# Kernel tuning notes

Measured on AMD Instinct MI355X. Metric: run time of the kernel, lower is better.

## Reference

```python
import jax, jax.numpy as jnp
import numpy as np

N, F, E = 100000, 128, 1600000


def setup_inputs() -> dict:
    key = jax.random.key(0)
    ks = jax.random.split(key, 10)
    s = 1.0 / np.sqrt(F)
    return {
        "x": jax.random.normal(ks[0], (N, F), jnp.float32),
        "edge_index": jax.random.randint(ks[1], (2, E), 0, N),
        "edge_weight": jax.random.uniform(ks[2], (E,), jnp.float32),
        # EvolveGCNO initial weight (1, F, F) -> squeezed to (F, F)
        "initial_weight": jax.random.normal(ks[3], (F, F), jnp.float32) * s,
        # torch.nn.GRU(F, F) params, gate order (r, z, n)
        "gru_w_ih": jax.random.uniform(ks[4], (3 * F, F), jnp.float32, -s, s),
        "gru_w_hh": jax.random.uniform(ks[5], (3 * F, F), jnp.float32, -s, s),
        "gru_b_ih": jax.random.uniform(ks[6], (3 * F,), jnp.float32, -s, s),
        "gru_b_hh": jax.random.uniform(ks[7], (3 * F,), jnp.float32, -s, s),
        # Linear(F, 1)
        "lin_w": jax.random.uniform(ks[8], (1, F), jnp.float32, -s, s),
        "lin_b": jax.random.uniform(ks[9], (1,), jnp.float32, -s, s),
    }


def _evolve_weight(W0, w_ih, w_hh, b_ih, b_hh):
    # One GRU step: input = W0 rows (batch=F), hidden = W0 rows (first call of EvolveGCNO)
    gi = W0 @ w_ih.T + b_ih  # (F, 3F)
    gh = W0 @ w_hh.T + b_hh
    i_r, i_z, i_n = jnp.split(gi, 3, axis=-1)
    h_r, h_z, h_n = jnp.split(gh, 3, axis=-1)
    r = jax.nn.sigmoid(i_r + h_r)
    z = jax.nn.sigmoid(i_z + h_z)
    n = jnp.tanh(i_n + r * h_n)
    return (1.0 - z) * n + z * W0  # (F, F)


def reference(x, edge_index, edge_weight, initial_weight, gru_w_ih, gru_w_hh,
              gru_b_ih, gru_b_hh, lin_w, lin_b):
    W = _evolve_weight(initial_weight, gru_w_ih, gru_w_hh, gru_b_ih, gru_b_hh)
    n_nodes = x.shape[0]
    row, col = edge_index[0], edge_index[1]  # source, target
    # gcn_norm: add self loops (weight 1), sym-normalize D^-1/2 (A+I) D^-1/2
    loop = jnp.arange(n_nodes)
    row = jnp.concatenate([row, loop])
    col = jnp.concatenate([col, loop])
    w = jnp.concatenate([edge_weight, jnp.ones((n_nodes,), x.dtype)])
    deg = jax.ops.segment_sum(w, col, num_segments=n_nodes)
    dinv = jnp.where(deg > 0, jax.lax.rsqrt(deg), 0.0)
    norm = dinv[row] * w * dinv[col]  # (E+N,)
    xw = x @ W  # (N, F)
    # gather at sources, weighted scatter-add at targets
    h = jax.ops.segment_sum(norm[:, None] * xw[row], col, num_segments=n_nodes)
    h = jax.nn.relu(h)
    return (h @ lin_w.T + lin_b)[:, 0]  # (N,)
```

## Files before the change

kernel.cpp:

```cpp
#include <hip/hip_runtime.h>

#define F 128
#define DEG_SCALE 16777216.0f
#define DEG_INV   (1.0f / 16777216.0f)
#define BUCK_BITS 7
#define BUCK_COLS 128
#define CAP 2304
#define EPT 8

typedef _Float16 half8 __attribute__((ext_vector_type(8)));
typedef float f32x4 __attribute__((ext_vector_type(4)));
typedef float f32x2 __attribute__((ext_vector_type(2)));

__global__ __launch_bounds__(256) void init_kernel(
    int* __restrict__ cursor, int NZ, int NBUK,
    const float* __restrict__ W0, const float* __restrict__ wih,
    const float* __restrict__ whh, const float* __restrict__ bih,
    const float* __restrict__ bhh, _Float16* __restrict__ WTh,
    int* __restrict__ offs, int N, int total) {
  __shared__ float w0row[2][F];
  int b = blockIdx.x;
  if (b < NZ) {
    int i = b * 256 + threadIdx.x;
    if (i < NBUK) cursor[i] = 0;
    if (b == 0 && threadIdx.x == 0) offs[N] = total;
    return;
  }
  int half = threadIdx.x >> 7;
  int j = threadIdx.x & 127;
  int i = (b - NZ) * 2 + half;
  w0row[half][j] = W0[i * F + j];
  __syncthreads();
  float ar = 0, az = 0, an = 0, br = 0, bz = 0, bn = 0;
  const float* wi_r = wih + (size_t)j * F;
  const float* wi_z = wih + (size_t)(j + F) * F;
  const float* wi_n = wih + (size_t)(j + 2 * F) * F;
  const float* wh_r = whh + (size_t)j * F;
  const float* wh_z = whh + (size_t)(j + F) * F;
  const float* wh_n = whh + (size_t)(j + 2 * F) * F;
#pragma unroll 4
  for (int k = 0; k < F; ++k) {
    float a = w0row[half][k];
    ar = fmaf(a, wi_r[k], ar);
    az = fmaf(a, wi_z[k], az);
    an = fmaf(a, wi_n[k], an);
    br = fmaf(a, wh_r[k], br);
    bz = fmaf(a, wh_z[k], bz);
    bn = fmaf(a, wh_n[k], bn);
  }
  float gr = ar + bih[j] + br + bhh[j];
  float gz = az + bih[j + F] + bz + bhh[j + F];
  float r = 1.f / (1.f + expf(-gr));
  float z = 1.f / (1.f + expf(-gz));
  float n = tanhf(an + bih[j + 2 * F] + r * (bn + bhh[j + 2 * F]));
  float v = (1.f - z) * n + z * w0row[half][j];
  WTh[j * F + i] = (_Float16)v;
}

__global__ __launch_bounds__(256) void gemm_bin(
    const float* __restrict__ x, const _Float16* __restrict__ WT,
    _Float16* __restrict__ xwh, int N, int NG,
    const int* __restrict__ erow, const int* __restrict__ ecol,
    const float* __restrict__ ew, int* __restrict__ cursor,
    uint2* __restrict__ binned, int E, int NBUK, int NBIN) {
  __shared__ int cnt_base[2048];
  int bi = blockIdx.x;
  if (bi % 3 == 2) {
    int bb = bi / 3;
    if (bb >= NBIN) return;
    int* cnt = cnt_base;
    int* base = cnt_base + 1024;
    int tid = threadIdx.x;
    for (int u = tid; u < 1024; u += 256) cnt[u] = 0;
    __syncthreads();
    int e0 = bb * (256 * EPT) + tid;
    int cc[EPT];
    int lrank[EPT];
#pragma unroll
    for (int k = 0; k < EPT; ++k) {
      int e = e0 + k * 256;
      if (e < E) {
        cc[k] = ecol[e];
        lrank[k] = atomicAdd(&cnt[cc[k] >> BUCK_BITS], 1);
      } else cc[k] = -1;
    }
    __syncthreads();
    for (int u = tid; u < NBUK; u += 256) {
      int cu = cnt[u];
      base[u] = cu ? atomicAdd(&cursor[u], cu) : 0;
    }
    __syncthreads();
#pragma unroll
    for (int k = 0; k < EPT; ++k) {
      if (cc[k] >= 0) {
        int e = e0 + k * 256;
        int bk = cc[k] >> BUCK_BITS;
        int pos = base[bk] + lrank[k];
        if (pos < CAP) {
          unsigned cl = (unsigned)(cc[k] & (BUCK_COLS - 1));
          binned[(size_t)bk * CAP + pos] =
              make_uint2((unsigned)erow[e] | (cl << 17), __float_as_uint(ew[e]));
        }
      }
    }
    return;
  }
  int g = (bi / 3) * 2 + (bi % 3);
  if (g >= NG) return;
  int t = threadIdx.x;
  int lane = t & 63, wave = t >> 6;
  int ln = lane & 15, q = lane >> 4;
  int rowb = g * 64 + wave * 16;
  int i = rowb + ln;
  int iclamp = (i < N) ? i : N - 1;
  const float* xp = x + (size_t)iclamp * F + q * 8;

  half8 a[4];
#pragma unroll
  for (int tt = 0; tt < 4; ++tt) {
    float4 v0 = *(const float4*)(xp + 32 * tt);
    float4 v1 = *(const float4*)(xp + 32 * tt + 4);
    half8 av;
    av[0] = (_Float16)v0.x; av[1] = (_Float16)v0.y;
    av[2] = (_Float16)v0.z; av[3] = (_Float16)v0.w;
    av[4] = (_Float16)v1.x; av[5] = (_Float16)v1.y;
    av[6] = (_Float16)v1.z; av[7] = (_Float16)v1.w;
    a[tt] = av;
  }

  f32x4 acc[8];
#pragma unroll
  for (int nt = 0; nt < 8; ++nt) acc[nt] = (f32x4){0.f, 0.f, 0.f, 0.f};

#pragma unroll
  for (int nt = 0; nt < 8; ++nt) {
#pragma unroll
    for (int tt = 0; tt < 4; ++tt) {
      half8 bfrag = *(const half8*)&WT[(size_t)(nt * 16 + ln) * F + tt * 32 + q * 8];
      acc[nt] = __builtin_amdgcn_mfma_f32_16x16x32_f16(a[tt], bfrag, acc[nt], 0, 0, 0);
    }
  }

#pragma unroll
  for (int nt = 0; nt < 8; ++nt) {
#pragma unroll
    for (int r = 0; r < 4; ++r) {
      int rowi = rowb + q * 4 + r;
      if (rowi < N) xwh[(size_t)rowi * F + nt * 16 + ln] = (_Float16)acc[nt][r];
    }
  }
}

__global__ __launch_bounds__(256) void csr_deg(
    const uint2* __restrict__ binned, const int* __restrict__ cursor,
    int* __restrict__ offs, float* __restrict__ dinv, int N, int NBUK) {
  __shared__ unsigned long long acc[BUCK_COLS];
  __shared__ int sc[BUCK_COLS];
  __shared__ int wsum[4];
  int b = blockIdx.x;
  int tid = threadIdx.x;
  if (tid < BUCK_COLS) acc[tid] = 0ull;
  int partial = 0;
  for (int i = tid; i < b; i += 256) partial += cursor[i];
#pragma unroll
  for (int m = 32; m; m >>= 1) partial += __shfl_xor(partial, m);
  if ((tid & 63) == 0) wsum[tid >> 6] = partial;
  __syncthreads();
  int bstart = b * BUCK_COLS + wsum[0] + wsum[1] + wsum[2] + wsum[3];

  int cnt = cursor[b];
  if (cnt > CAP) cnt = CAP;
  const uint2* src = binned + (size_t)b * CAP;
  for (int i = tid; i < cnt; i += 256) {
    uint2 rec = src[i];
    int cl = rec.x >> 17;
    unsigned fx = (unsigned)(__uint_as_float(rec.y) * DEG_SCALE);
    atomicAdd(&acc[cl], ((unsigned long long)1 << 32) | (unsigned long long)fx);
  }
  __syncthreads();
  int node0 = b * BUCK_COLS;
  int cvt1 = 0;
  if (tid < BUCK_COLS) {
    unsigned long long pk = acc[tid];
    int node = node0 + tid;
    if (node < N) {
      cvt1 = (int)(pk >> 32) + 1;
      float deg = (float)(unsigned)(pk & 0xffffffffull) * DEG_INV;
      float dv = rsqrtf(deg + 1.0f);
      dinv[node] = dv;
    }
    sc[tid] = cvt1;
  }
  __syncthreads();
  for (int off = 1; off < BUCK_COLS; off <<= 1) {
    int xv = 0;
    if (tid < BUCK_COLS && tid >= off) xv = sc[tid - off];
    __syncthreads();
    if (tid < BUCK_COLS) sc[tid] += xv;
    __syncthreads();
  }
  if (tid < BUCK_COLS) {
    int node = node0 + tid;
    if (node < N) offs[node] = bstart + sc[tid] - cvt1;
  }
}

__global__ __launch_bounds__(256) void csr_pairs(
    const uint2* __restrict__ binned, const int* __restrict__ cursor,
    const int* __restrict__ offs, const float* __restrict__ dinv,
    uint2* __restrict__ pairs, int N, int NBUK) {
  __shared__ float dinvL[BUCK_COLS];
  __shared__ int wbase[BUCK_COLS];
  int b = blockIdx.x;
  int tid = threadIdx.x;
  int node0 = b * BUCK_COLS;
  if (tid < BUCK_COLS) {
    int node = node0 + tid;
    if (node < N) {
      int o = offs[node];
      float dv = dinv[node];
      dinvL[tid] = dv;
      wbase[tid] = o + 1;
      pairs[o] = make_uint2((unsigned)node << 8, __float_as_uint(dv * dv));
    }
  }
  __syncthreads();
  int cnt = cursor[b];
  if (cnt > CAP) cnt = CAP;
  const uint2* src = binned + (size_t)b * CAP;
  for (int i = tid; i < cnt; i += 256) {
    uint2 rec = src[i];
    int cl = rec.x >> 17;
    unsigned r = rec.x & 0x1ffffu;
    float wp = (__uint_as_float(rec.y) * dinvL[cl]) * dinv[r];
    int pos = atomicAdd(&wbase[cl], 1);
    pairs[pos] = make_uint2(r << 8, __float_as_uint(wp));
  }
}

__global__ __launch_bounds__(256) void gather_out(
    const uint2* __restrict__ pairs, const int* __restrict__ offs,
    const char* __restrict__ xwb, const float* __restrict__ linw,
    const float* __restrict__ linb, float* __restrict__ out, int N) {
  int wave = threadIdx.x >> 6;
  int lane = threadIdx.x & 63;
  int node = blockIdx.x * 4 + wave;
  if (node >= N) return;
  int c = lane & 15;
  int q = lane >> 4;

  const char* xb = xwb + (c << 4);
  f32x2 acc[4];
#pragma unroll
  for (int j = 0; j < 4; ++j) acc[j] = (f32x2){0.f, 0.f};

  int start = offs[node], end = offs[node + 1];
  for (int it = start + q; it < end; it += 16) {
    int i1 = (it + 4 < end) ? it + 4 : it;
    int i2 = (it + 8 < end) ? it + 8 : it;
    int i3 = (it + 12 < end) ? it + 12 : it;
    uint2 p0 = pairs[it];
    uint2 p1 = pairs[i1];
    uint2 p2 = pairs[i2];
    uint2 p3 = pairs[i3];
    float n0 = __uint_as_float(p0.y);
    float n1 = (it + 4 < end) ? __uint_as_float(p1.y) : 0.f;
    float n2 = (it + 8 < end) ? __uint_as_float(p2.y) : 0.f;
    float n3 = (it + 12 < end) ? __uint_as_float(p3.y) : 0.f;
    half8 x0 = *(const half8*)(xb + p0.x);
    half8 x1 = *(const half8*)(xb + p1.x);
    half8 x2 = *(const half8*)(xb + p2.x);
    half8 x3 = *(const half8*)(xb + p3.x);
    f32x2 nv0 = {n0, n0}, nv1 = {n1, n1}, nv2 = {n2, n2}, nv3 = {n3, n3};
#pragma unroll
    for (int j = 0; j < 4; ++j) {
      f32x2 v; v[0] = (float)x0[2 * j]; v[1] = (float)x0[2 * j + 1];
      acc[j] += nv0 * v;
    }
#pragma unroll
    for (int j = 0; j < 4; ++j) {
      f32x2 v; v[0] = (float)x1[2 * j]; v[1] = (float)x1[2 * j + 1];
      acc[j] += nv1 * v;
    }
#pragma unroll
    for (int j = 0; j < 4; ++j) {
      f32x2 v; v[0] = (float)x2[2 * j]; v[1] = (float)x2[2 * j + 1];
      acc[j] += nv2 * v;
    }
#pragma unroll
    for (int j = 0; j < 4; ++j) {
      f32x2 v; v[0] = (float)x3[2 * j]; v[1] = (float)x3[2 * j + 1];
      acc[j] += nv3 * v;
    }
  }

  float a8[8];
#pragma unroll
  for (int j = 0; j < 8; ++j) a8[j] = acc[j >> 1][j & 1];
#pragma unroll
  for (int j = 0; j < 8; ++j) {
    a8[j] += __shfl_xor(a8[j], 16);
    a8[j] += __shfl_xor(a8[j], 32);
  }

  const float4* lw4 = (const float4*)linw;
  float4 la = lw4[c * 2];
  float4 lb = lw4[c * 2 + 1];
  float p = fmaxf(a8[0], 0.f) * la.x + fmaxf(a8[1], 0.f) * la.y +
            fmaxf(a8[2], 0.f) * la.z + fmaxf(a8[3], 0.f) * la.w +
            fmaxf(a8[4], 0.f) * lb.x + fmaxf(a8[5], 0.f) * lb.y +
            fmaxf(a8[6], 0.f) * lb.z + fmaxf(a8[7], 0.f) * lb.w;
#pragma unroll
  for (int m = 8; m; m >>= 1) p += __shfl_xor(p, m);

  if (lane == 0) out[node] = p + linb[0];
}

extern "C" void kernel_launch(void* const* d_in, const int* in_sizes, int n_in,
                              void* d_out, int out_size, void* d_ws, size_t ws_size,
                              hipStream_t stream) {
  const float* x    = (const float*)d_in[0];
  const int*   ei   = (const int*)d_in[1];
  const float* ew   = (const float*)d_in[2];
  const float* W0   = (const float*)d_in[3];
  const float* wih  = (const float*)d_in[4];
  const float* whh  = (const float*)d_in[5];
  const float* bih  = (const float*)d_in[6];
  const float* bhh  = (const float*)d_in[7];
  const float* linw = (const float*)d_in[8];
  const float* linb = (const float*)d_in[9];

  int N = in_sizes[0] / F;
  int E = in_sizes[2];
  const int* row = ei;
  const int* col = ei + E;
  int NBUK = (N + BUCK_COLS - 1) / BUCK_COLS;
  int total = E + N;

  char* p = (char*)d_ws;
  auto alloc = [&](size_t bytes) {
    char* q = p;
    p += (bytes + 255) & ~(size_t)255;
    return q;
  };
  _Float16* WTh    = (_Float16*)alloc((size_t)F * F * 2);
  int*      cursor = (int*)alloc((size_t)NBUK * 4);
  float*    dinv   = (float*)alloc((size_t)N * 4);
  int*      offs   = (int*)alloc(((size_t)N + 1) * 4);
  uint2*    binned = (uint2*)alloc((size_t)NBUK * CAP * 8);
  uint2*    pairs  = (uint2*)alloc(((size_t)total + 16) * 8);
  _Float16* xwh    = (_Float16*)alloc((size_t)N * F * 2);

  int NZ = (NBUK + 255) / 256;
  init_kernel<<<NZ + 64, 256, 0, stream>>>(cursor, NZ, NBUK, W0, wih, whh, bih, bhh,
                                           WTh, offs, N, total);

  int NG = (N + 63) / 64;
  int NBIN = (E + 256 * EPT - 1) / (256 * EPT);
  int half_g = (NG + 1) / 2;
  int G3 = NBIN > half_g ? NBIN : half_g;
  gemm_bin<<<3 * G3, 256, 0, stream>>>(x, WTh, xwh, N, NG, row, col, ew, cursor,
                                       binned, E, NBUK, NBIN);

  csr_deg<<<NBUK, 256, 0, stream>>>(binned, cursor, offs, dinv, N, NBUK);
  csr_pairs<<<NBUK, 256, 0, stream>>>(binned, cursor, offs, dinv, pairs, N, NBUK);

  gather_out<<<(N + 3) / 4, 256, 0, stream>>>(pairs, offs, (const char*)xwh,
                                              linw, linb, (float*)d_out, N);
}
```

Baseline: 267.8 us.

## Fuse degree accumulation into gemm_bin via global atomics and co-schedule GEMM with binning

```diff
diff --git a/kernel.cpp b/kernel.cpp
--- a/kernel.cpp
+++ b/kernel.cpp
@@ -6,14 +6,15 @@
 #define BUCK_BITS 7
 #define BUCK_COLS 128
 #define CAP 2304
-#define EPT 8
+#define EPB 2048
 
 typedef _Float16 half8 __attribute__((ext_vector_type(8)));
 typedef float f32x4 __attribute__((ext_vector_type(4)));
 typedef float f32x2 __attribute__((ext_vector_type(2)));
 
 __global__ __launch_bounds__(256) void init_kernel(
-    int* __restrict__ cursor, int NZ, int NBUK,
+    int* __restrict__ cursor, unsigned long long* __restrict__ deg64,
+    int NZ, int NBUK,
     const float* __restrict__ W0, const float* __restrict__ wih,
     const float* __restrict__ whh, const float* __restrict__ bih,
     const float* __restrict__ bhh, _Float16* __restrict__ WTh,
@@ -22,6 +23,7 @@
   int b = blockIdx.x;
   if (b < NZ) {
     int i = b * 256 + threadIdx.x;
+    if (i < N) deg64[i] = 0ull;
     if (i < NBUK) cursor[i] = 0;
     if (b == 0 && threadIdx.x == 0) offs[N] = total;
     return;
@@ -57,109 +59,111 @@
   WTh[j * F + i] = (_Float16)v;
 }
 
-__global__ __launch_bounds__(256) void gemm_bin(
+__global__ __launch_bounds__(512) void gemm_bin(
     const float* __restrict__ x, const _Float16* __restrict__ WT,
-    _Float16* __restrict__ xwh, int N, int NG,
+    _Float16* __restrict__ xwh, int N,
     const int* __restrict__ erow, const int* __restrict__ ecol,
     const float* __restrict__ ew, int* __restrict__ cursor,
-    uint2* __restrict__ binned, int E, int NBUK, int NBIN) {
-  __shared__ int cnt_base[2048];
+    unsigned long long* __restrict__ deg64, uint2* __restrict__ binned,
+    int E, int NBUK) {
+  __shared__ int cnt[1024];
+  __shared__ int base[1024];
   int bi = blockIdx.x;
-  if (bi % 3 == 2) {
-    int bb = bi / 3;
-    if (bb >= NBIN) return;
-    int* cnt = cnt_base;
-    int* base = cnt_base + 1024;
-    int tid = threadIdx.x;
-    for (int u = tid; u < 1024; u += 256) cnt[u] = 0;
-    __syncthreads();
-    int e0 = bb * (256 * EPT) + tid;
-    int cc[EPT];
-    int lrank[EPT];
-#pragma unroll
-    for (int k = 0; k < EPT; ++k) {
-      int e = e0 + k * 256;
-      if (e < E) {
-        cc[k] = ecol[e];
-        lrank[k] = atomicAdd(&cnt[cc[k] >> BUCK_BITS], 1);
-      } else cc[k] = -1;
-    }
-    __syncthreads();
-    for (int u = tid; u < NBUK; u += 256) {
-      int cu = cnt[u];
-      base[u] = cu ? atomicAdd(&cursor[u], cu) : 0;
-    }
-    __syncthreads();
-#pragma unroll
-    for (int k = 0; k < EPT; ++k) {
-      if (cc[k] >= 0) {
-        int e = e0 + k * 256;
-        int bk = cc[k] >> BUCK_BITS;
-        int pos = base[bk] + lrank[k];
-        if (pos < CAP) {
-          unsigned cl = (unsigned)(cc[k] & (BUCK_COLS - 1));
-          binned[(size_t)bk * CAP + pos] =
-              make_uint2((unsigned)erow[e] | (cl << 17), __float_as_uint(ew[e]));
-        }
+  int tid = threadIdx.x;
+
+  int e0 = bi * EPB + tid;
+  int cc[4];
+  unsigned rr[4];
+  float wv[4];
+#pragma unroll
+  for (int k = 0; k < 4; ++k) {
+    int e = e0 + k * 512;
+    if (e < E) {
+      cc[k] = ecol[e];
+      rr[k] = (unsigned)erow[e];
+      wv[k] = ew[e];
+    } else cc[k] = -1;
+  }
+#pragma unroll
+  for (int k = 0; k < 4; ++k) {
+    if (cc[k] >= 0) {
+      unsigned fx = (unsigned)(wv[k] * DEG_SCALE);
+      atomicAdd(&deg64[cc[k]],
+                ((unsigned long long)1 << 32) | (unsigned long long)fx);
+    }
+  }
+  for (int u = tid; u < 1024; u += 512) cnt[u] = 0;
+
+  int lane = tid & 63, wave = tid >> 6;
+  int ln = lane & 15, q = lane >> 4;
+  int rowb0 = bi * 128;
+  if (rowb0 < N) {
+    int n = wave * 16 + ln;
+    half8 bfr[4];
+#pragma unroll
+    for (int tt = 0; tt < 4; ++tt)
+      bfr[tt] = *(const half8*)&WT[(size_t)n * F + tt * 32 + q * 8];
+    for (int rt = 0; rt < 8; ++rt) {
+      int rowb = rowb0 + rt * 16;
+      int i = rowb + ln;
+      int iclamp = (i < N) ? i : N - 1;
+      const float* xp = x + (size_t)iclamp * F + q * 8;
+      half8 a[4];
+#pragma unroll
+      for (int tt = 0; tt < 4; ++tt) {
+        float4 v0 = *(const float4*)(xp + 32 * tt);
+        float4 v1 = *(const float4*)(xp + 32 * tt + 4);
+        half8 av;
+        av[0] = (_Float16)v0.x; av[1] = (_Float16)v0.y;
+        av[2] = (_Float16)v0.z; av[3] = (_Float16)v0.w;
+        av[4] = (_Float16)v1.x; av[5] = (_Float16)v1.y;
+        av[6] = (_Float16)v1.z; av[7] = (_Float16)v1.w;
+        a[tt] = av;
       }
-    }
-    return;
-  }
-  int g = (bi / 3) * 2 + (bi % 3);
-  if (g >= NG) return;
-  int t = threadIdx.x;
-  int lane = t & 63, wave = t >> 6;
-  int ln = lane & 15, q = lane >> 4;
-  int rowb = g * 64 + wave * 16;
-  int i = rowb + ln;
-  int iclamp = (i < N) ? i : N - 1;
-  const float* xp = x + (size_t)iclamp * F + q * 8;
-
-  half8 a[4];
-#pragma unroll
-  for (int tt = 0; tt < 4; ++tt) {
-    float4 v0 = *(const float4*)(xp + 32 * tt);
-    float4 v1 = *(const float4*)(xp + 32 * tt + 4);
-    half8 av;
-    av[0] = (_Float16)v0.x; av[1] = (_Float16)v0.y;
-    av[2] = (_Float16)v0.z; av[3] = (_Float16)v0.w;
-    av[4] = (_Float16)v1.x; av[5] = (_Float16)v1.y;
-    av[6] = (_Float16)v1.z; av[7] = (_Float16)v1.w;
-    a[tt] = av;
-  }
-
-  f32x4 acc[8];
-#pragma unroll
-  for (int nt = 0; nt < 8; ++nt) acc[nt] = (f32x4){0.f, 0.f, 0.f, 0.f};
-
-#pragma unroll
-  for (int nt = 0; nt < 8; ++nt) {
-#pragma unroll
-    for (int tt = 0; tt < 4; ++tt) {
-      half8 bfrag = *(const half8*)&WT[(size_t)(nt * 16 + ln) * F + tt * 32 + q * 8];
-      acc[nt] = __builtin_amdgcn_mfma_f32_16x16x32_f16(a[tt], bfrag, acc[nt], 0, 0, 0);
-    }
-  }
-
-#pragma unroll
-  for (int nt = 0; nt < 8; ++nt) {
-#pragma unroll
-    for (int r = 0; r < 4; ++r) {
-      int rowi = rowb + q * 4 + r;
-      if (rowi < N) xwh[(size_t)rowi * F + nt * 16 + ln] = (_Float16)acc[nt][r];
-    }
-  }
-}
-
-__global__ __launch_bounds__(256) void csr_deg(
-    const uint2* __restrict__ binned, const int* __restrict__ cursor,
+      f32x4 acc = (f32x4){0.f, 0.f, 0.f, 0.f};
+#pragma unroll
+      for (int tt = 0; tt < 4; ++tt)
+        acc = __builtin_amdgcn_mfma_f32_16x16x32_f16(a[tt], bfr[tt], acc, 0, 0, 0);
+#pragma unroll
+      for (int r = 0; r < 4; ++r) {
+        int rowi = rowb + q * 4 + r;
+        if (rowi < N) xwh[(size_t)rowi * F + n] = (_Float16)acc[r];
+      }
+    }
+  }
+
+  __syncthreads();
+  int lrank[4];
+#pragma unroll
+  for (int k = 0; k < 4; ++k)
+    if (cc[k] >= 0) lrank[k] = atomicAdd(&cnt[cc[k] >> BUCK_BITS], 1);
+  __syncthreads();
+  for (int u = tid; u < NBUK; u += 512) {
+    int cu = cnt[u];
+    base[u] = cu ? atomicAdd(&cursor[u], cu) : 0;
+  }
+  __syncthreads();
+#pragma unroll
+  for (int k = 0; k < 4; ++k) {
+    if (cc[k] >= 0) {
+      int bk = cc[k] >> BUCK_BITS;
+      int pos = base[bk] + lrank[k];
+      if (pos < CAP) {
+        unsigned cl = (unsigned)(cc[k] & (BUCK_COLS - 1));
+        binned[(size_t)bk * CAP + pos] =
+            make_uint2(rr[k] | (cl << 17), __float_as_uint(wv[k]));
+      }
+    }
+  }
+}
+
+__global__ __launch_bounds__(256) void node_kernel(
+    const unsigned long long* __restrict__ deg64, const int* __restrict__ cursor,
     int* __restrict__ offs, float* __restrict__ dinv, int N, int NBUK) {
-  __shared__ unsigned long long acc[BUCK_COLS];
   __shared__ int sc[BUCK_COLS];
   __shared__ int wsum[4];
   int b = blockIdx.x;
   int tid = threadIdx.x;
-  if (tid < BUCK_COLS) acc[tid] = 0ull;
   int partial = 0;
   for (int i = tid; i < b; i += 256) partial += cursor[i];
 #pragma unroll
@@ -168,22 +172,12 @@
   __syncthreads();
   int bstart = b * BUCK_COLS + wsum[0] + wsum[1] + wsum[2] + wsum[3];
 
-  int cnt = cursor[b];
-  if (cnt > CAP) cnt = CAP;
-  const uint2* src = binned + (size_t)b * CAP;
-  for (int i = tid; i < cnt; i += 256) {
-    uint2 rec = src[i];
-    int cl = rec.x >> 17;
-    unsigned fx = (unsigned)(__uint_as_float(rec.y) * DEG_SCALE);
-    atomicAdd(&acc[cl], ((unsigned long long)1 << 32) | (unsigned long long)fx);
-  }
-  __syncthreads();
   int node0 = b * BUCK_COLS;
   int cvt1 = 0;
   if (tid < BUCK_COLS) {
-    unsigned long long pk = acc[tid];
     int node = node0 + tid;
     if (node < N) {
+      unsigned long long pk = deg64[node];
       cvt1 = (int)(pk >> 32) + 1;
       float deg = (float)(unsigned)(pk & 0xffffffffull) * DEG_INV;
       float dv = rsqrtf(deg + 1.0f);
@@ -345,24 +339,24 @@
   };
   _Float16* WTh    = (_Float16*)alloc((size_t)F * F * 2);
   int*      cursor = (int*)alloc((size_t)NBUK * 4);
+  unsigned long long* deg64 = (unsigned long long*)alloc((size_t)N * 8);
   float*    dinv   = (float*)alloc((size_t)N * 4);
   int*      offs   = (int*)alloc(((size_t)N + 1) * 4);
   uint2*    binned = (uint2*)alloc((size_t)NBUK * CAP * 8);
   uint2*    pairs  = (uint2*)alloc(((size_t)total + 16) * 8);
   _Float16* xwh    = (_Float16*)alloc((size_t)N * F * 2);
 
-  int NZ = (NBUK + 255) / 256;
-  init_kernel<<<NZ + 64, 256, 0, stream>>>(cursor, NZ, NBUK, W0, wih, whh, bih, bhh,
-                                           WTh, offs, N, total);
-
-  int NG = (N + 63) / 64;
-  int NBIN = (E + 256 * EPT - 1) / (256 * EPT);
-  int half_g = (NG + 1) / 2;
-  int G3 = NBIN > half_g ? NBIN : half_g;
-  gemm_bin<<<3 * G3, 256, 0, stream>>>(x, WTh, xwh, N, NG, row, col, ew, cursor,
-                                       binned, E, NBUK, NBIN);
-
-  csr_deg<<<NBUK, 256, 0, stream>>>(binned, cursor, offs, dinv, N, NBUK);
+  int NZ = (N + 255) / 256;
+  init_kernel<<<NZ + 64, 256, 0, stream>>>(cursor, deg64, NZ, NBUK, W0, wih, whh,
+                                           bih, bhh, WTh, offs, N, total);
+
+  int NROW = (N + 127) / 128;
+  int NBIN = (E + EPB - 1) / EPB;
+  int NB = NROW > NBIN ? NROW : NBIN;
+  gemm_bin<<<NB, 512, 0, stream>>>(x, WTh, xwh, N, row, col, ew, cursor,
+                                   deg64, binned, E, NBUK);
+
+  node_kernel<<<NBUK, 256, 0, stream>>>(deg64, cursor, offs, dinv, N, NBUK);
   csr_pairs<<<NBUK, 256, 0, stream>>>(binned, cursor, offs, dinv, pairs, N, NBUK);
 
   gather_out<<<(N + 3) / 4, 256, 0, stream>>>(pairs, offs, (const char*)xwh,
```

New measurement: 330.4 us. 1.23x slower.
